# Performance work log

Measured on AMD Instinct MI355X. Metric: run time of the kernel, lower is better.

Reference implementation:

```python
import jax, jax.numpy as jnp
import numpy as np

B, T, H = 16, 512, 1024
L, D = 8192, 256

def setup_inputs() -> dict:
    key = jax.random.key(0)
    k1, k2, k3, k4, k5 = jax.random.split(key, 5)
    X = jax.random.normal(k1, (B, T, H), dtype=jnp.float32)
    attention_mask = jnp.ones((B, T), dtype=jnp.int32)
    queries = jax.random.normal(k2, (L, D), dtype=jnp.float32) * 0.02
    Wk = jax.random.normal(k3, (D, H), dtype=jnp.float32) * (1.0 / np.sqrt(H))
    Wv = jax.random.normal(k4, (D, H), dtype=jnp.float32) * (1.0 / np.sqrt(H))
    out_weight = jax.random.normal(k5, (L, D), dtype=jnp.float32) * 0.02
    out_bias = jnp.zeros((L,), dtype=jnp.float32)
    return {"X": X, "attention_mask": attention_mask, "queries": queries,
            "Wk": Wk, "Wv": Wv, "out_weight": out_weight, "out_bias": out_bias}

def reference(X, attention_mask, queries, Wk, Wv, out_weight, out_bias):
    # K, V: [B, T, D] (nn.Linear with weight [D, H], no bias)
    K = jnp.einsum('bth,dh->btd', X, Wk)
    V = jnp.einsum('bth,dh->btd', X, Wv)
    scale = 1.0 / jnp.sqrt(jnp.asarray(K.shape[-1], dtype=K.dtype))
    # attention logits: [B, L, T]
    attn_logits = jnp.einsum('ld,btd->blt', queries, K) * scale
    neg = jnp.finfo(attn_logits.dtype).min
    attn_logits = jnp.where(attention_mask[:, None, :] == 0, neg, attn_logits)
    attn = jax.nn.softmax(attn_logits, axis=-1)
    # per-label context: [B, L, D]
    ctx = jnp.einsum('blt,btd->bld', attn, V)
    # fused per-label output projection: [B, L]
    logits = jnp.einsum('bld,ld->bl', ctx, out_weight) + out_bias[None, :]
    return logits
```

## Files before the change

### kernel.cpp

```cpp
#include <hip/hip_runtime.h>
#include <hip/hip_bf16.h>


typedef __bf16 bf16x8 __attribute__((ext_vector_type(8)));
typedef float f32x4 __attribute__((ext_vector_type(4)));

__device__ __forceinline__ unsigned short f2bf(float f) {
    unsigned int u = __builtin_bit_cast(unsigned int, f);
    unsigned int lsb = (u >> 16) & 1u;
    u += 0x7fffu + lsb;
    return (unsigned short)(u >> 16);
}

__device__ __forceinline__ void gld_lds16(const void* g, void* l) {
    __builtin_amdgcn_global_load_lds((__attribute__((address_space(1))) void*)g,
                                     (__attribute__((address_space(3))) void*)l,
                                     16, 0, 0);
}

__global__ __launch_bounds__(256) void cvt_all(const float* __restrict__ X,
                                               const float* __restrict__ Q,
                                               const float* __restrict__ Wo,
                                               const float* __restrict__ Wk,
                                               const float* __restrict__ Wv,
                                               unsigned short* __restrict__ dst) {
    int base = blockIdx.x * 1024 + threadIdx.x;
#pragma unroll
    for (int r = 0; r < 4; ++r) {
        int idx = base + r * 256;
        const float* src;
        int off;
        float s = 1.0f;
        if (idx < 2097152)      { src = X;  off = idx; }
        else if (idx < 2621440) { src = Q;  off = idx - 2097152; s = 0.09016844006f; }
        else if (idx < 3145728) { src = Wo; off = idx - 2621440; }
        else if (idx < 3211264) { src = Wk; off = idx - 3145728; }
        else                    { src = Wv; off = idx - 3211264; }
        float4 v = ((const float4*)src)[off];
        ushort4 o;
        o.x = f2bf(v.x * s); o.y = f2bf(v.y * s);
        o.z = f2bf(v.z * s); o.w = f2bf(v.w * s);
        ((ushort4*)dst)[idx] = o;
    }
}

__global__ __launch_bounds__(256) void kv_gemm(const unsigned short* __restrict__ Xb,
                                               const unsigned short* __restrict__ Wb,
                                               unsigned short* __restrict__ Kb,
                                               unsigned short* __restrict__ Vb) {
    __shared__ unsigned short Xs[128 * 72];
    __shared__ unsigned short Ws[128 * 72];
    const int bid = blockIdx.x;
    const int nt = bid & 3, mt = bid >> 2;
    const int m0 = mt * 128, n0 = nt * 128;
    const int tid = threadIdx.x;
    const int lane = tid & 63, w = tid >> 6;
    const int q = lane >> 4, ln = lane & 15;
    const int wm = (w & 1) * 64, wn = (w >> 1) * 64;

    f32x4 acc[4][4];
#pragma unroll
    for (int mi = 0; mi < 4; ++mi)
#pragma unroll
        for (int ni = 0; ni < 4; ++ni) acc[mi][ni] = f32x4{0.f, 0.f, 0.f, 0.f};

#pragma unroll 1
    for (int h0 = 0; h0 < 1024; h0 += 64) {
#pragma unroll
        for (int i = 0; i < 4; ++i) {
            int c = tid + i * 256;
            int row = c >> 3, off = (c & 7) << 3;
            *(uint4*)(&Xs[row * 72 + off]) = *(const uint4*)(&Xb[(m0 + row) * 1024 + h0 + off]);
            *(uint4*)(&Ws[row * 72 + off]) = *(const uint4*)(&Wb[(n0 + row) * 1024 + h0 + off]);
        }
        __syncthreads();
#pragma unroll
        for (int ks = 0; ks < 64; ks += 32) {
            bf16x8 a[4], b[4];
#pragma unroll
            for (int mi = 0; mi < 4; ++mi)
                a[mi] = *(const bf16x8*)(&Xs[(wm + mi * 16 + ln) * 72 + ks + q * 8]);
#pragma unroll
            for (int ni = 0; ni < 4; ++ni)
                b[ni] = *(const bf16x8*)(&Ws[(wn + ni * 16 + ln) * 72 + ks + q * 8]);
#pragma unroll
            for (int mi = 0; mi < 4; ++mi)
#pragma unroll
                for (int ni = 0; ni < 4; ++ni)
                    acc[mi][ni] = __builtin_amdgcn_mfma_f32_16x16x32_bf16(
                        a[mi], b[ni], acc[mi][ni], 0, 0, 0);
        }
        __syncthreads();
    }
    {
        unsigned short* dst = (n0 < 256) ? Kb : Vb;
        const int d0 = (n0 & 255) + wn;
#pragma unroll
        for (int mi = 0; mi < 4; ++mi)
#pragma unroll
            for (int ni = 0; ni < 4; ++ni) {
                int d = d0 + ni * 16 + ln;
#pragma unroll
                for (int r = 0; r < 4; ++r) {
                    int m = m0 + wm + mi * 16 + q * 4 + r;
                    dst[m * 256 + d] = f2bf(acc[mi][ni][r]);
                }
            }
    }
}

__global__ __launch_bounds__(256, 2) void attn_fused(const unsigned short* __restrict__ Qb,
                                                     const unsigned short* __restrict__ Wob,
                                                     const unsigned short* __restrict__ Kb,
                                                     const unsigned short* __restrict__ Vb,
                                                     const int* __restrict__ mask,
                                                     const float* __restrict__ bias,
                                                     float* __restrict__ out) {
    __shared__ unsigned short Ks[2][8192];
    __shared__ unsigned short Vs[2][8192];
    const int bid = blockIdx.x;
    const int bb = bid >> 6;
    const int l0 = (bid & 63) * 128;
    const int tid = threadIdx.x;
    const int lane = tid & 63, w = tid >> 6;
    const int q = lane >> 4, ln = lane & 15;
    const int hi = lane >> 5, lo = lane & 31;

    auto stage = [&](int c) {
        const int p = c & 1;
        const int rbase = bb * 512 + c * 32;
#pragma unroll
        for (int j = 0; j < 8; ++j) {
            int gid = w * 8 + j;
            int g = gid & 15;
            const unsigned short* srcb = (gid < 16) ? Kb : Vb;
            unsigned short* dstb = (gid < 16) ? &Ks[p][0] : &Vs[p][0];
            int tl = 2 * g + hi;
            gld_lds16(srcb + (size_t)(rbase + tl) * 256 + ((lo ^ tl) << 3),
                      dstb + g * 512);
        }
    };
    stage(0);

    unsigned mbits = 0;
    {
        const int* mrow = mask + bb * 512;
#pragma unroll
        for (int j = 0; j < 32; ++j)
            mbits |= (mrow[j * 16 + ln] != 0 ? 1u : 0u) << j;
    }

    bf16x8 aQ[2][8], aW[2][8];
#pragma unroll
    for (int mi = 0; mi < 2; ++mi) {
        const int row = (l0 + w * 32 + mi * 16 + ln) * 256;
#pragma unroll
        for (int kk = 0; kk < 8; ++kk) {
            aQ[mi][kk] = *(const bf16x8*)(&Qb[row + kk * 32 + q * 8]);
            aW[mi][kk] = *(const bf16x8*)(&Wob[row + kk * 32 + q * 8]);
        }
    }

    float num[2][4], den[2][4];
#pragma unroll
    for (int mi = 0; mi < 2; ++mi)
#pragma unroll
        for (int r = 0; r < 4; ++r) { num[mi][r] = 0.f; den[mi][r] = 0.f; }

#pragma unroll 1
    for (int c = 0; c < 16; ++c) {
        asm volatile("s_waitcnt vmcnt(0)" ::: "memory");
        __syncthreads();
        if (c < 15) stage(c + 1);
        const int p = c & 1;

        f32x4 Sa[2][2], Pa[2][2];
#pragma unroll
        for (int mi = 0; mi < 2; ++mi)
#pragma unroll
            for (int ni = 0; ni < 2; ++ni) {
                Sa[mi][ni] = f32x4{0.f, 0.f, 0.f, 0.f};
                Pa[mi][ni] = f32x4{0.f, 0.f, 0.f, 0.f};
            }

#pragma unroll
        for (int kk = 0; kk < 8; ++kk) {
            bf16x8 bK[2], bV[2];
#pragma unroll
            for (int ni = 0; ni < 2; ++ni) {
                const int t = ni * 16 + ln;
                const int off = t * 256 + (((kk * 4 + q) ^ t) << 3);
                bK[ni] = *(const bf16x8*)(&Ks[p][off]);
                bV[ni] = *(const bf16x8*)(&Vs[p][off]);
            }
#pragma unroll
            for (int mi = 0; mi < 2; ++mi)
#pragma unroll
                for (int ni = 0; ni < 2; ++ni) {
                    Sa[mi][ni] = __builtin_amdgcn_mfma_f32_16x16x32_bf16(
                        aQ[mi][kk], bK[ni], Sa[mi][ni], 0, 0, 0);
                    Pa[mi][ni] = __builtin_amdgcn_mfma_f32_16x16x32_bf16(
                        aW[mi][kk], bV[ni], Pa[mi][ni], 0, 0, 0);
                }
        }
#pragma unroll
        for (int ni = 0; ni < 2; ++ni) {
            bool ok = (mbits >> (c * 2 + ni)) & 1u;
#pragma unroll
            for (int mi = 0; mi < 2; ++mi)
#pragma unroll
                for (int r = 0; r < 4; ++r) {
                    float e = ok ? __builtin_amdgcn_exp2f(Sa[mi][ni][r]) : 0.0f;
                    den[mi][r] += e;
                    num[mi][r] += e * Pa[mi][ni][r];
                }
        }
    }

#pragma unroll
    for (int mi = 0; mi < 2; ++mi)
#pragma unroll
        for (int r = 0; r < 4; ++r) {
            float n_ = num[mi][r], d_ = den[mi][r];
#pragma unroll
            for (int o = 1; o < 16; o <<= 1) {
                n_ += __shfl_xor(n_, o);
                d_ += __shfl_xor(d_, o);
            }
            if (ln == 0) {
                int l = l0 + w * 32 + mi * 16 + q * 4 + r;
                out[bb * 8192 + l] = n_ / d_ + bias[l];
            }
        }
}

extern "C" void kernel_launch(void* const* d_in, const int* in_sizes, int n_in,
                              void* d_out, int out_size, void* d_ws, size_t ws_size,
                              hipStream_t stream) {
    const float* X    = (const float*)d_in[0];
    const int*   mask = (const int*)d_in[1];
    const float* Q    = (const float*)d_in[2];
    const float* Wk   = (const float*)d_in[3];
    const float* Wv   = (const float*)d_in[4];
    const float* Wo   = (const float*)d_in[5];
    const float* bias = (const float*)d_in[6];
    float* out = (float*)d_out;

    unsigned short* Xb   = (unsigned short*)d_ws;
    unsigned short* Qb   = Xb + 8388608ull;
    unsigned short* Wob  = Qb + 2097152ull;
    unsigned short* Wkvb = Wob + 2097152ull;
    unsigned short* Kb   = Wkvb + 524288ull;
    unsigned short* Vb   = Kb + 2097152ull;

    cvt_all<<<dim3(3200), 256, 0, stream>>>(X, Q, Wo, Wk, Wv, Xb);
    kv_gemm<<<dim3(256), 256, 0, stream>>>(Xb, Wkvb, Kb, Vb);
    attn_fused<<<dim3(1024), 256, 0, stream>>>(Qb, Wob, Kb, Vb, mask, bias, out);
}
```

Before: 191.3 us.

## Read K/V fragments directly from global memory instead of LDS staging

Removes the double-buffered LDS staging of K and V tiles (global_load_lds plus barriers) and has each lane load its MFMA B-operand fragments straight from global memory. This drops the per-chunk __syncthreads and the LDS footprint, which may allow more resident blocks. In exchange, every wave re-fetches the same K/V rows through the cache hierarchy, and the loads are no longer prefetched one chunk ahead, so latency may be exposed.

Result: slower. 362.0 us (+89.2%).

```diff
diff --git a/kernel.cpp b/kernel.cpp
--- a/kernel.cpp
+++ b/kernel.cpp
@@ -10,12 +10,6 @@
     unsigned int lsb = (u >> 16) & 1u;
     u += 0x7fffu + lsb;
     return (unsigned short)(u >> 16);
-}
-
-__device__ __forceinline__ void gld_lds16(const void* g, void* l) {
-    __builtin_amdgcn_global_load_lds((__attribute__((address_space(1))) void*)g,
-                                     (__attribute__((address_space(3))) void*)l,
-                                     16, 0, 0);
 }
 
 __global__ __launch_bounds__(256) void cvt_all(const float* __restrict__ X,
@@ -116,31 +110,12 @@
                                                      const int* __restrict__ mask,
                                                      const float* __restrict__ bias,
                                                      float* __restrict__ out) {
-    __shared__ unsigned short Ks[2][8192];
-    __shared__ unsigned short Vs[2][8192];
     const int bid = blockIdx.x;
     const int bb = bid >> 6;
     const int l0 = (bid & 63) * 128;
     const int tid = threadIdx.x;
     const int lane = tid & 63, w = tid >> 6;
     const int q = lane >> 4, ln = lane & 15;
-    const int hi = lane >> 5, lo = lane & 31;
-
-    auto stage = [&](int c) {
-        const int p = c & 1;
-        const int rbase = bb * 512 + c * 32;
-#pragma unroll
-        for (int j = 0; j < 8; ++j) {
-            int gid = w * 8 + j;
-            int g = gid & 15;
-            const unsigned short* srcb = (gid < 16) ? Kb : Vb;
-            unsigned short* dstb = (gid < 16) ? &Ks[p][0] : &Vs[p][0];
-            int tl = 2 * g + hi;
-            gld_lds16(srcb + (size_t)(rbase + tl) * 256 + ((lo ^ tl) << 3),
-                      dstb + g * 512);
-        }
-    };
-    stage(0);
 
     unsigned mbits = 0;
     {
@@ -161,6 +136,10 @@
         }
     }
 
+    const size_t bbase = ((size_t)(bb * 512 + ln)) * 256 + q * 8;
+    const unsigned short* __restrict__ pK = Kb + bbase;
+    const unsigned short* __restrict__ pV = Vb + bbase;
+
     float num[2][4], den[2][4];
 #pragma unroll
     for (int mi = 0; mi < 2; ++mi)
@@ -169,10 +148,7 @@
 
 #pragma unroll 1
     for (int c = 0; c < 16; ++c) {
-        asm volatile("s_waitcnt vmcnt(0)" ::: "memory");
-        __syncthreads();
-        if (c < 15) stage(c + 1);
-        const int p = c & 1;
+        const int coff = c * 32 * 256;
 
         f32x4 Sa[2][2], Pa[2][2];
 #pragma unroll
@@ -188,10 +164,9 @@
             bf16x8 bK[2], bV[2];
 #pragma unroll
             for (int ni = 0; ni < 2; ++ni) {
-                const int t = ni * 16 + ln;
-                const int off = t * 256 + (((kk * 4 + q) ^ t) << 3);
-                bK[ni] = *(const bf16x8*)(&Ks[p][off]);
-                bV[ni] = *(const bf16x8*)(&Vs[p][off]);
+                const int off = coff + ni * 16 * 256 + kk * 32;
+                bK[ni] = *(const bf16x8*)(&pK[off]);
+                bV[ni] = *(const bf16x8*)(&pV[off]);
             }
 #pragma unroll
             for (int mi = 0; mi < 2; ++mi)
```

## Double-buffer KV GEMM tiles with direct global-to-LDS loads and XOR swizzle

Applied to the files above, without the earlier changes.

The K/V projection GEMM now stages its X and W tiles into two LDS buffers using global_load_lds, so the next chunk's loads are issued before the current chunk's MFMAs and overlap with them. The padded LDS layout is replaced by an XOR swizzle on 16-byte groups to avoid bank conflicts, since direct LDS loads cannot write padded rows. Doubling the LDS buffers raises shared memory per block, which may reduce occupancy. The full vmcnt(0) wait at the top of each iteration limits how much overlap is possible.

Result: no change. 192.2 us (+0.5%).

```diff
diff --git a/kernel.cpp b/kernel.cpp
--- a/kernel.cpp
+++ b/kernel.cpp
@@ -48,8 +48,8 @@
                                                const unsigned short* __restrict__ Wb,
                                                unsigned short* __restrict__ Kb,
                                                unsigned short* __restrict__ Vb) {
-    __shared__ unsigned short Xs[128 * 72];
-    __shared__ unsigned short Ws[128 * 72];
+    __shared__ unsigned short Xs[2][128 * 64];
+    __shared__ unsigned short Ws[2][128 * 64];
     const int bid = blockIdx.x;
     const int nt = bid & 3, mt = bid >> 2;
     const int m0 = mt * 128, n0 = nt * 128;
@@ -57,6 +57,8 @@
     const int lane = tid & 63, w = tid >> 6;
     const int q = lane >> 4, ln = lane & 15;
     const int wm = (w & 1) * 64, wn = (w >> 1) * 64;
+    const int lrow = lane >> 3;
+    const int gsw  = (lane & 7) ^ lrow;
 
     f32x4 acc[4][4];
 #pragma unroll
@@ -64,25 +66,42 @@
 #pragma unroll
         for (int ni = 0; ni < 4; ++ni) acc[mi][ni] = f32x4{0.f, 0.f, 0.f, 0.f};
 
+    auto stage = [&](int hc) {
+        const int p = hc & 1;
+        const int h0 = hc * 64;
+#pragma unroll
+        for (int j = 0; j < 4; ++j) {
+            int slot = w * 4 + j;
+            int r = slot * 8 + lrow;
+            gld_lds16(Xb + (size_t)(m0 + r) * 1024 + h0 + gsw * 8,
+                      &Xs[p][slot * 512]);
+            gld_lds16(Wb + (size_t)(n0 + r) * 1024 + h0 + gsw * 8,
+                      &Ws[p][slot * 512]);
+        }
+    };
+    stage(0);
+
 #pragma unroll 1
-    for (int h0 = 0; h0 < 1024; h0 += 64) {
-#pragma unroll
-        for (int i = 0; i < 4; ++i) {
-            int c = tid + i * 256;
-            int row = c >> 3, off = (c & 7) << 3;
-            *(uint4*)(&Xs[row * 72 + off]) = *(const uint4*)(&Xb[(m0 + row) * 1024 + h0 + off]);
-            *(uint4*)(&Ws[row * 72 + off]) = *(const uint4*)(&Wb[(n0 + row) * 1024 + h0 + off]);
-        }
+    for (int hc = 0; hc < 16; ++hc) {
+        asm volatile("s_waitcnt vmcnt(0)" ::: "memory");
         __syncthreads();
+        if (hc < 15) stage(hc + 1);
+        const int p = hc & 1;
 #pragma unroll
         for (int ks = 0; ks < 64; ks += 32) {
             bf16x8 a[4], b[4];
 #pragma unroll
-            for (int mi = 0; mi < 4; ++mi)
-                a[mi] = *(const bf16x8*)(&Xs[(wm + mi * 16 + ln) * 72 + ks + q * 8]);
-#pragma unroll
-            for (int ni = 0; ni < 4; ++ni)
-                b[ni] = *(const bf16x8*)(&Ws[(wn + ni * 16 + ln) * 72 + ks + q * 8]);
+            for (int mi = 0; mi < 4; ++mi) {
+                int r = wm + mi * 16 + ln;
+                int g = ((ks >> 3) + q) ^ (r & 7);
+                a[mi] = *(const bf16x8*)(&Xs[p][r * 64 + g * 8]);
+            }
+#pragma unroll
+            for (int ni = 0; ni < 4; ++ni) {
+                int r = wn + ni * 16 + ln;
+                int g = ((ks >> 3) + q) ^ (r & 7);
+                b[ni] = *(const bf16x8*)(&Ws[p][r * 64 + g * 8]);
+            }
 #pragma unroll
             for (int mi = 0; mi < 4; ++mi)
 #pragma unroll
```
